# Kernel tuning notes

Hardware: AMD Instinct MI355X
Metric: run time of the kernel (lower is better)

The kernel has to match this reference:

```python
import jax, jax.numpy as jnp
import numpy as np

T, H, E, F, K, FS = 2048, 2048, 64, 512, 8, 512


def setup_inputs() -> dict:
    key = jax.random.key(0)
    ks = jax.random.split(key, 6)
    s = 0.02
    return {
        "hidden_states": jax.random.normal(ks[0], (T, H), jnp.float32),
        # merged gate: E router logits + 1 shared-expert gate logit
        "W_gate": jax.random.normal(ks[1], (H, E + 1), jnp.float32) * s,
        # per-expert merged gate_up proj: [E, H, 2F]
        "W_gate_up": jax.random.normal(ks[2], (E, H, 2 * F), jnp.float32) * s,
        "W_down": jax.random.normal(ks[3], (E, F, H), jnp.float32) * s,
        # shared expert
        "Ws_gate_up": jax.random.normal(ks[4], (H, 2 * FS), jnp.float32) * s,
        "Ws_down": jax.random.normal(ks[5], (FS, H), jnp.float32) * s,
    }


def reference(hidden_states, W_gate, W_gate_up, W_down, Ws_gate_up, Ws_down):
    x = hidden_states  # [T, H]
    logits_all = x @ W_gate                      # [T, E+1]
    router_logits = logits_all[:, :E]
    shared_gate_logit = logits_all[:, E:]        # [T, 1]

    # FusedMoE routing: softmax -> top_k -> renormalize (norm_topk_prob=True)
    probs = jax.nn.softmax(router_logits.astype(jnp.float32), axis=-1)
    topk_w, topk_idx = jax.lax.top_k(probs, K)   # [T, K]
    topk_w = topk_w / jnp.sum(topk_w, axis=-1, keepdims=True)
    # dense combine weights [T, E] (zero for unselected experts)
    combine = jnp.zeros((T, E), probs.dtype).at[
        jnp.arange(T)[:, None], topk_idx].set(topk_w)

    # grouped expert GEMMs (dense reference: every expert sees all tokens,
    # combine-weights zero-out unrouted pairs)
    gu = jnp.einsum('th,ehf->etf', x, W_gate_up)   # [E, T, 2F]
    g, u = jnp.split(gu, 2, axis=-1)
    act = jax.nn.silu(g) * u                       # [E, T, F]
    # apply combine weight before down-proj to avoid [E, T, H] intermediate
    act = act * combine.T[:, :, None].astype(act.dtype)
    routed = jnp.einsum('etf,efh->th', act, W_down)  # [T, H]

    # shared expert (Qwen3NextMLP with sigmoid expert_gate)
    sgu = x @ Ws_gate_up                           # [T, 2FS]
    sg, su = jnp.split(sgu, 2, axis=-1)
    shared = (jax.nn.silu(sg) * su) @ Ws_down      # [T, H]
    shared = jax.nn.sigmoid(shared_gate_logit) * shared

    return shared + routed.astype(x.dtype)
```

## Files before the change

### kernel.cpp

```cpp
#include <hip/hip_runtime.h>
#include <hip/hip_bf16.h>
#include <math.h>

#define T_TOK 2048
#define H_DIM 2048
#define E_NUM 64
#define F_DIM 512
#define K_TOP 8
#define FS_DIM 512
#define NROWS (T_TOK * K_TOP)

typedef __attribute__((ext_vector_type(8))) short short8v;
typedef __attribute__((ext_vector_type(4))) float f32x4;

static __device__ __forceinline__ unsigned short f2bf(float f) {
    unsigned int u = __float_as_uint(f);
    u += 0x7fff + ((u >> 16) & 1);
    return (unsigned short)(u >> 16);
}

#define BCHUNK(row, k8) ((((k8) ^ ((row) + ((row) >> 3)))) & 7)
#define ASWZ(row) (((row) + ((row) >> 3)) & 7)

typedef const unsigned int __attribute__((address_space(1))) gu32;
typedef unsigned int __attribute__((address_space(3))) lu32;
#define GLDS16(gsrc, ldst) \
    __builtin_amdgcn_global_load_lds((gu32*)(gsrc), (lu32*)(ldst), 16, 0, 0)

__global__ __launch_bounds__(256) void cvt_bf16_kernel(
    const float* __restrict__ in, unsigned short* __restrict__ out, int n8)
{
    int i = blockIdx.x * 256 + threadIdx.x;
    if (i < n8) {
        const float4* p = (const float4*)(in + (size_t)i * 8);
        float4 v0 = p[0], v1 = p[1];
        ushort4 a = make_ushort4(f2bf(v0.x), f2bf(v0.y), f2bf(v0.z), f2bf(v0.w));
        ushort4 b = make_ushort4(f2bf(v1.x), f2bf(v1.y), f2bf(v1.z), f2bf(v1.w));
        ushort4* q = (ushort4*)(out + (size_t)i * 8);
        q[0] = a; q[1] = b;
    }
}

__global__ __launch_bounds__(64) void router_kernel(
    const float* __restrict__ x, const float* __restrict__ Wg,
    int* __restrict__ topk_idx, float* __restrict__ topk_w,
    float* __restrict__ sgate, int* __restrict__ counts)
{
    const int t = blockIdx.x;
    const int lane = threadIdx.x;
    const float* xr = x + (size_t)t * H_DIM;

    float a0 = 0.f, a1 = 0.f, a2 = 0.f, a3 = 0.f;
    for (int h = 0; h < H_DIM; h += 4) {
        float4 xv = *(const float4*)&xr[h];
        a0 += xv.x * Wg[(h + 0) * 65 + lane];
        a1 += xv.y * Wg[(h + 1) * 65 + lane];
        a2 += xv.z * Wg[(h + 2) * 65 + lane];
        a3 += xv.w * Wg[(h + 3) * 65 + lane];
    }
    float logit = (a0 + a1) + (a2 + a3);

    float a64 = 0.f;
    for (int h = lane; h < H_DIM; h += 64) a64 += xr[h] * Wg[h * 65 + 64];
#pragma unroll
    for (int off = 32; off >= 1; off >>= 1) a64 += __shfl_xor(a64, off);

    float v = logit;
    float selv[K_TOP]; int seli[K_TOP];
#pragma unroll
    for (int k = 0; k < K_TOP; ++k) {
        float mv = v; int mi = lane;
#pragma unroll
        for (int off = 32; off >= 1; off >>= 1) {
            float ov = __shfl_xor(mv, off);
            int   oi = __shfl_xor(mi, off);
            if (ov > mv || (ov == mv && oi < mi)) { mv = ov; mi = oi; }
        }
        selv[k] = mv; seli[k] = mi;
        if (lane == mi) v = -INFINITY;
    }

    if (lane == 0) {
        float m = selv[0];
        float w[K_TOP]; float s = 0.f;
#pragma unroll
        for (int k = 0; k < K_TOP; ++k) { w[k] = __expf(selv[k] - m); s += w[k]; }
        float inv = 1.f / s;
#pragma unroll
        for (int k = 0; k < K_TOP; ++k) {
            topk_idx[t * K_TOP + k] = seli[k];
            topk_w[t * K_TOP + k] = w[k] * inv;
            atomicAdd(&counts[seli[k]], 1);
        }
        sgate[t] = 1.f / (1.f + __expf(-a64));
    }
}

__global__ __launch_bounds__(256) void bucket_kernel(
    const int* __restrict__ topk_idx, const float* __restrict__ topk_w,
    const int* __restrict__ counts, int* __restrict__ offsets,
    int* __restrict__ bucket_tok, float* __restrict__ bucket_w)
{
    const int e = blockIdx.x, thr = threadIdx.x;
    __shared__ int cnt[256];
    __shared__ int base_s;
    const int q0 = thr * 64;
    int c = 0;
    for (int q = 0; q < 64; ++q) c += (topk_idx[q0 + q] == e) ? 1 : 0;
    cnt[thr] = c;
    __syncthreads();
    if (thr == 0) {
        int off = 0;
        for (int i = 0; i < e; ++i) off += counts[i];
        offsets[e] = off;
        base_s = off;
        int run = 0;
        for (int i = 0; i < 256; ++i) { int tval = cnt[i]; cnt[i] = run; run += tval; }
    }
    __syncthreads();
    int pos = base_s + cnt[thr];
    for (int q = 0; q < 64; ++q) {
        int pp = q0 + q;
        if (topk_idx[pp] == e) {
            bucket_tok[pos] = pp >> 3;
            bucket_w[pos] = topk_w[pp];
            ++pos;
        }
    }
}

template<bool ROUTED>
__global__ __launch_bounds__(256, 2) void gu_mfma_kernel(
    const unsigned short* __restrict__ xb,
    const float* __restrict__ Wall,
    const int* __restrict__ counts, const int* __restrict__ offsets,
    const int* __restrict__ bucket_tok, const float* __restrict__ bucket_w,
    unsigned short* __restrict__ actout)
{
    constexpr int BM = 128;
    __shared__ __align__(16) unsigned short As[2][BM * 64];
    __shared__ __align__(16) unsigned short Bs[2][128 * 64];
    __shared__ int   toksS[BM];
    __shared__ float twsS[BM];

    const int tid  = threadIdx.x;
    const int lane = tid & 63;
    const int wid  = tid >> 6;
    const int wm = wid >> 1, wn = wid & 1;
    const int lrow = lane & 15, lhi = lane >> 4;

    int cblk, ne, base;
    const float* W;
    if (ROUTED) {
        int nw = (blockIdx.x & 7) * ((int)gridDim.x >> 3) + (blockIdx.x >> 3);
        int e = nw >> 3; cblk = nw & 7;
        ne = counts[e]; base = offsets[e];
        W = Wall + (size_t)e * H_DIM * (2 * F_DIM);
    } else {
        cblk = blockIdx.x;
        ne = T_TOK; base = 0;
        W = Wall;
    }
    const int c0 = cblk * 64;

    const int n4 = (tid & 31) * 4;
    const int kq = (tid >> 5) * 8;
    const int grp = n4 >> 5;
    const int srccol = c0 + (grp >> 1) * 32 + (n4 & 31) + ((grp & 1) ? F_DIM : 0);
    int wrB[4];
#pragma unroll
    for (int cc = 0; cc < 4; ++cc) {
        int n = n4 + cc;
        wrB[cc] = n * 64 + BCHUNK(n, kq >> 3) * 8;
    }
    int rdB[4][2];
#pragma unroll
    for (int fn = 0; fn < 4; ++fn) {
        int r = wn * 64 + fn * 16 + lrow;
#pragma unroll
        for (int ks = 0; ks < 2; ++ks) {
            int kc = ks * 4 + lhi;
            rdB[fn][ks] = r * 64 + BCHUNK(r, kc) * 8;
        }
    }
    int rdA[4][2];
#pragma unroll
    for (int fm = 0; fm < 4; ++fm) {
        int arow = wm * 64 + fm * 16 + lrow;
#pragma unroll
        for (int ks = 0; ks < 2; ++ks) {
            int kc = ks * 4 + lhi;
            rdA[fm][ks] = arow * 64 + ((kc ^ ASWZ(arow)) & 7) * 8;
        }
    }
    const int NT = H_DIM / 64;

    const int m0_beg = ROUTED ? 0 : blockIdx.y * BM;
    const int m0_end = ROUTED ? ne : m0_beg + BM;

    for (int m0 = m0_beg; m0 < m0_end; m0 += BM) {
        __syncthreads();
        if (tid < BM) {
            int idx = m0 + tid; bool v = idx < ne;
            if (ROUTED) {
                toksS[tid] = v ? bucket_tok[base + idx] : bucket_tok[base];
                twsS[tid]  = v ? bucket_w[base + idx] : 0.f;
            } else {
                toksS[tid] = v ? idx : (T_TOK - 1);
                twsS[tid]  = 1.f;
            }
        }
        __syncthreads();

        int asrc[4];
#pragma unroll
        for (int i = 0; i < 4; ++i) {
            int row = wid * 32 + i * 8 + (lane >> 3);
            asrc[i] = toksS[row] * H_DIM + (((lane & 7) ^ ASWZ(row)) << 3);
        }

        f32x4 acc[4][4];
#pragma unroll
        for (int i = 0; i < 4; ++i)
#pragma unroll
            for (int j = 0; j < 4; ++j) acc[i][j] = (f32x4){0.f, 0.f, 0.f, 0.f};

        float4 bq[8];
#pragma unroll
        for (int j = 0; j < 8; ++j)
            bq[j] = *(const float4*)&W[(size_t)(kq + j) * (2 * F_DIM) + srccol];
#pragma unroll
        for (int cc = 0; cc < 4; ++cc) {
            short8v pk;
#pragma unroll
            for (int j = 0; j < 8; ++j)
                pk[j] = (short)f2bf(((const float*)&bq[j])[cc]);
            *(short8v*)&Bs[0][wrB[cc]] = pk;
        }
#pragma unroll
        for (int j = 0; j < 8; ++j)
            bq[j] = *(const float4*)&W[(size_t)(64 + kq + j) * (2 * F_DIM) + srccol];
#pragma unroll
        for (int i = 0; i < 4; ++i)
            GLDS16(xb + asrc[i], &As[0][(wid * 32 + i * 8) * 64]);
        __syncthreads();

        for (int kt = 0; kt < NT; ++kt) {
            const int k0 = kt * 64;
            if (kt + 1 < NT) {
#pragma unroll
                for (int i = 0; i < 4; ++i)
                    GLDS16(xb + asrc[i] + k0 + 64, &As[(kt + 1) & 1][(wid * 32 + i * 8) * 64]);
                unsigned short* nB = Bs[(kt + 1) & 1];
#pragma unroll
                for (int cc = 0; cc < 4; ++cc) {
                    short8v pk;
#pragma unroll
                    for (int j = 0; j < 8; ++j)
                        pk[j] = (short)f2bf(((const float*)&bq[j])[cc]);
                    *(short8v*)&nB[wrB[cc]] = pk;
                }
                int knx = (kt + 2 < NT) ? (k0 + 128) : (k0 + 64);
#pragma unroll
                for (int j = 0; j < 8; ++j)
                    bq[j] = *(const float4*)&W[(size_t)(knx + kq + j) * (2 * F_DIM) + srccol];
            }
            __builtin_amdgcn_sched_barrier(0);
            const unsigned short* A_ = As[kt & 1];
            const unsigned short* B_ = Bs[kt & 1];
#pragma unroll
            for (int ks = 0; ks < 2; ++ks) {
                short8v bf[4];
#pragma unroll
                for (int fn = 0; fn < 4; ++fn) bf[fn] = *(const short8v*)&B_[rdB[fn][ks]];
#pragma unroll
                for (int fm = 0; fm < 4; ++fm) {
                    short8v af = *(const short8v*)&A_[rdA[fm][ks]];
#pragma unroll
                    for (int fn = 0; fn < 4; ++fn)
                        acc[fm][fn] = __builtin_amdgcn_mfma_f32_16x16x32_bf16(
                            af, bf[fn], acc[fm][fn], 0, 0, 0);
                }
            }
            __syncthreads();
        }

#pragma unroll
        for (int fm = 0; fm < 4; ++fm) {
#pragma unroll
            for (int p = 0; p < 2; ++p) {
                const int acol = c0 + wn * 32 + p * 16 + lrow;
#pragma unroll
                for (int i = 0; i < 4; ++i) {
                    int ml = wm * 64 + fm * 16 + lhi * 4 + i;
                    int idx = m0 + ml;
                    if (idx < ne) {
                        float gv = acc[fm][p][i], uv = acc[fm][p + 2][i];
                        float sg = gv / (1.f + __expf(-gv));
                        float val = sg * uv * twsS[ml];
                        size_t orow = ROUTED ? (size_t)(base + idx) : (size_t)idx;
                        actout[orow * F_DIM + acol] = f2bf(val);
                    }
                }
            }
        }
    }
}

template<bool ROUTED>
__global__ __launch_bounds__(256, 2) void down_mfma_kernel(
    const unsigned short* __restrict__ actb,
    const float* __restrict__ Wall,
    const int* __restrict__ counts, const int* __restrict__ offsets,
    const int* __restrict__ bucket_tok, const float* __restrict__ sgate,
    float* __restrict__ out)
{
    constexpr int BM = 128;
    __shared__ __align__(16) unsigned short As[2][BM * 64];
    __shared__ __align__(16) unsigned short Bs[2][128 * 64];
    __shared__ int   toksS[BM];
    __shared__ float sgS[BM];

    const int tid  = threadIdx.x;
    const int lane = tid & 63;
    const int wid  = tid >> 6;
    const int wm = wid >> 1, wn = wid & 1;
    const int lrow = lane & 15, lhi = lane >> 4;

    int cblk, ne, base;
    const float* W;
    if (ROUTED) {
        int nw = (blockIdx.x & 7) * ((int)gridDim.x >> 3) + (blockIdx.x >> 3);
        int e = nw >> 4; cblk = nw & 15;
        ne = counts[e]; base = offsets[e];
        W = Wall + (size_t)e * F_DIM * H_DIM;
    } else {
        cblk = blockIdx.x;
        ne = T_TOK; base = 0;
        W = Wall;
    }
    const int c0 = cblk * 128;

    const int n4 = (tid & 31) * 4;
    const int kq = (tid >> 5) * 8;
    const int srccol = c0 + n4;
    int wrB[4];
#pragma unroll
    for (int cc = 0; cc < 4; ++cc) {
        int n = n4 + cc;
        wrB[cc] = n * 64 + BCHUNK(n, kq >> 3) * 8;
    }
    int rdB[4][2];
#pragma unroll
    for (int fn = 0; fn < 4; ++fn) {
        int r = wn * 64 + fn * 16 + lrow;
#pragma unroll
        for (int ks = 0; ks < 2; ++ks) {
            int kc = ks * 4 + lhi;
            rdB[fn][ks] = r * 64 + BCHUNK(r, kc) * 8;
        }
    }
    int rdA[4][2];
#pragma unroll
    for (int fm = 0; fm < 4; ++fm) {
        int arow = wm * 64 + fm * 16 + lrow;
#pragma unroll
        for (int ks = 0; ks < 2; ++ks) {
            int kc = ks * 4 + lhi;
            rdA[fm][ks] = arow * 64 + ((kc ^ ASWZ(arow)) & 7) * 8;
        }
    }
    const int NT = F_DIM / 64;

    const int m0_beg = ROUTED ? 0 : blockIdx.y * BM;
    const int m0_end = ROUTED ? ne : m0_beg + BM;

    for (int m0 = m0_beg; m0 < m0_end; m0 += BM) {
        __syncthreads();
        if (tid < BM) {
            int idx = m0 + tid;
            if (ROUTED) {
                toksS[tid] = (idx < ne) ? bucket_tok[base + idx] : 0;
            } else {
                sgS[tid] = sgate[(idx < ne) ? idx : (T_TOK - 1)];
            }
        }
        __syncthreads();

        int asrc[4];
#pragma unroll
        for (int i = 0; i < 4; ++i) {
            int row = wid * 32 + i * 8 + (lane >> 3);
            int grow = ROUTED ? min(base + m0 + row, NROWS - 1)
                              : min(m0 + row, T_TOK - 1);
            asrc[i] = grow * F_DIM + (((lane & 7) ^ ASWZ(row)) << 3);
        }

        f32x4 acc[4][4];
#pragma unroll
        for (int i = 0; i < 4; ++i)
#pragma unroll
            for (int j = 0; j < 4; ++j) acc[i][j] = (f32x4){0.f, 0.f, 0.f, 0.f};

        float4 bq[8];
#pragma unroll
        for (int j = 0; j < 8; ++j)
            bq[j] = *(const float4*)&W[(size_t)(kq + j) * H_DIM + srccol];
#pragma unroll
        for (int cc = 0; cc < 4; ++cc) {
            short8v pk;
#pragma unroll
            for (int j = 0; j < 8; ++j)
                pk[j] = (short)f2bf(((const float*)&bq[j])[cc]);
            *(short8v*)&Bs[0][wrB[cc]] = pk;
        }
#pragma unroll
        for (int j = 0; j < 8; ++j)
            bq[j] = *(const float4*)&W[(size_t)(64 + kq + j) * H_DIM + srccol];
#pragma unroll
        for (int i = 0; i < 4; ++i)
            GLDS16(actb + asrc[i], &As[0][(wid * 32 + i * 8) * 64]);
        __syncthreads();

        for (int kt = 0; kt < NT; ++kt) {
            const int k0 = kt * 64;
            if (kt + 1 < NT) {
#pragma unroll
                for (int i = 0; i < 4; ++i)
                    GLDS16(actb + asrc[i] + k0 + 64, &As[(kt + 1) & 1][(wid * 32 + i * 8) * 64]);
                unsigned short* nB = Bs[(kt + 1) & 1];
#pragma unroll
                for (int cc = 0; cc < 4; ++cc) {
                    short8v pk;
#pragma unroll
                    for (int j = 0; j < 8; ++j)
                        pk[j] = (short)f2bf(((const float*)&bq[j])[cc]);
                    *(short8v*)&nB[wrB[cc]] = pk;
                }
                int knx = (kt + 2 < NT) ? (k0 + 128) : (k0 + 64);
#pragma unroll
                for (int j = 0; j < 8; ++j)
                    bq[j] = *(const float4*)&W[(size_t)(knx + kq + j) * H_DIM + srccol];
            }
            __builtin_amdgcn_sched_barrier(0);
            const unsigned short* A_ = As[kt & 1];
            const unsigned short* B_ = Bs[kt & 1];
#pragma unroll
            for (int ks = 0; ks < 2; ++ks) {
                short8v bf[4];
#pragma unroll
                for (int fn = 0; fn < 4; ++fn) bf[fn] = *(const short8v*)&B_[rdB[fn][ks]];
#pragma unroll
                for (int fm = 0; fm < 4; ++fm) {
                    short8v af = *(const short8v*)&A_[rdA[fm][ks]];
#pragma unroll
                    for (int fn = 0; fn < 4; ++fn)
                        acc[fm][fn] = __builtin_amdgcn_mfma_f32_16x16x32_bf16(
                            af, bf[fn], acc[fm][fn], 0, 0, 0);
                }
            }
            __syncthreads();
        }

#pragma unroll
        for (int fm = 0; fm < 4; ++fm) {
#pragma unroll
            for (int fn = 0; fn < 4; ++fn) {
                int col = c0 + wn * 64 + fn * 16 + lrow;
#pragma unroll
                for (int i = 0; i < 4; ++i) {
                    int ml = wm * 64 + fm * 16 + lhi * 4 + i;
                    int idx = m0 + ml;
                    if (idx < ne) {
                        if (ROUTED)
                            atomicAdd(&out[(size_t)toksS[ml] * H_DIM + col], acc[fm][fn][i]);
                        else
                            out[(size_t)idx * H_DIM + col] = sgS[ml] * acc[fm][fn][i];
                    }
                }
            }
        }
    }
}

extern "C" void kernel_launch(void* const* d_in, const int* in_sizes, int n_in,
                              void* d_out, int out_size, void* d_ws, size_t ws_size,
                              hipStream_t stream) {
    const float* x    = (const float*)d_in[0];
    const float* Wg   = (const float*)d_in[1];
    const float* Wgu  = (const float*)d_in[2];
    const float* Wd   = (const float*)d_in[3];
    const float* Wsgu = (const float*)d_in[4];
    const float* Wsd  = (const float*)d_in[5];
    float* out = (float*)d_out;

    char* p = (char*)d_ws;
    auto alloc = [&](size_t bytes) {
        char* r = p;
        p += (bytes + 255) & ~(size_t)255;
        return r;
    };
    int*   topk_idx   = (int*)  alloc((size_t)T_TOK * K_TOP * sizeof(int));
    float* topk_w     = (float*)alloc((size_t)T_TOK * K_TOP * sizeof(float));
    float* sgate      = (float*)alloc((size_t)T_TOK * sizeof(float));
    int*   counts     = (int*)  alloc((size_t)E_NUM * sizeof(int));
    int*   offsets    = (int*)  alloc((size_t)E_NUM * sizeof(int));
    int*   bucket_tok = (int*)  alloc((size_t)NROWS * sizeof(int));
    float* bucket_w   = (float*)alloc((size_t)NROWS * sizeof(float));
    unsigned short* xb    = (unsigned short*)alloc((size_t)T_TOK * H_DIM * 2);
    unsigned short* act_r = (unsigned short*)alloc((size_t)NROWS * F_DIM * 2);
    unsigned short* act_s = (unsigned short*)alloc((size_t)T_TOK * FS_DIM * 2);

    hipMemsetAsync(counts, 0, E_NUM * sizeof(int), stream);
    cvt_bf16_kernel<<<(T_TOK * H_DIM / 8 + 255) / 256, 256, 0, stream>>>(x, xb, T_TOK * H_DIM / 8);
    router_kernel<<<T_TOK, 64, 0, stream>>>(x, Wg, topk_idx, topk_w, sgate, counts);
    bucket_kernel<<<E_NUM, 256, 0, stream>>>(topk_idx, topk_w, counts, offsets, bucket_tok, bucket_w);

    gu_mfma_kernel<true><<<8 * E_NUM, 256, 0, stream>>>(
        xb, Wgu, counts, offsets, bucket_tok, bucket_w, act_r);
    gu_mfma_kernel<false><<<dim3(8, T_TOK / 128), 256, 0, stream>>>(
        xb, Wsgu, counts, offsets, bucket_tok, bucket_w, act_s);

    down_mfma_kernel<false><<<dim3(16, T_TOK / 128), 256, 0, stream>>>(
        act_s, Wsd, counts, offsets, bucket_tok, sgate, out);
    down_mfma_kernel<true><<<16 * E_NUM, 256, 0, stream>>>(
        act_r, Wd, counts, offsets, bucket_tok, sgate, out);
}
```

Baseline: 705.7 us.

## Merge shared and routed expert GEMMs into single launches per stage

```diff
diff --git a/kernel.cpp b/kernel.cpp
--- a/kernel.cpp
+++ b/kernel.cpp
@@ -129,13 +129,12 @@
     }
 }
 
-template<bool ROUTED>
 __global__ __launch_bounds__(256, 2) void gu_mfma_kernel(
     const unsigned short* __restrict__ xb,
-    const float* __restrict__ Wall,
+    const float* __restrict__ Wgu, const float* __restrict__ Wsgu,
     const int* __restrict__ counts, const int* __restrict__ offsets,
     const int* __restrict__ bucket_tok, const float* __restrict__ bucket_w,
-    unsigned short* __restrict__ actout)
+    unsigned short* __restrict__ act_r, unsigned short* __restrict__ act_s)
 {
     constexpr int BM = 128;
     __shared__ __align__(16) unsigned short As[2][BM * 64];
@@ -149,17 +148,20 @@
     const int wm = wid >> 1, wn = wid & 1;
     const int lrow = lane & 15, lhi = lane >> 4;
 
-    int cblk, ne, base;
+    const int nw  = (blockIdx.x & 7) * 80 + (blockIdx.x >> 3);
+    const int cblk = nw & 7;
+    const int eu   = nw >> 3;
+    const bool sh  = (eu >= E_NUM);
+    int ne, base, m0_beg, m0_end;
     const float* W;
-    if (ROUTED) {
-        int nw = (blockIdx.x & 7) * ((int)gridDim.x >> 3) + (blockIdx.x >> 3);
-        int e = nw >> 3; cblk = nw & 7;
-        ne = counts[e]; base = offsets[e];
-        W = Wall + (size_t)e * H_DIM * (2 * F_DIM);
+    if (sh) {
+        ne = T_TOK; base = 0;
+        m0_beg = (eu - E_NUM) * BM; m0_end = m0_beg + BM;
+        W = Wsgu;
     } else {
-        cblk = blockIdx.x;
-        ne = T_TOK; base = 0;
-        W = Wall;
+        ne = counts[eu]; base = offsets[eu];
+        m0_beg = 0; m0_end = ne;
+        W = Wgu + (size_t)eu * H_DIM * (2 * F_DIM);
     }
     const int c0 = cblk * 64;
 
@@ -195,19 +197,14 @@
     }
     const int NT = H_DIM / 64;
 
-    const int m0_beg = ROUTED ? 0 : blockIdx.y * BM;
-    const int m0_end = ROUTED ? ne : m0_beg + BM;
-
     for (int m0 = m0_beg; m0 < m0_end; m0 += BM) {
         __syncthreads();
         if (tid < BM) {
             int idx = m0 + tid; bool v = idx < ne;
-            if (ROUTED) {
+            if (sh) { toksS[tid] = v ? idx : (T_TOK - 1); twsS[tid] = 1.f; }
+            else {
                 toksS[tid] = v ? bucket_tok[base + idx] : bucket_tok[base];
                 twsS[tid]  = v ? bucket_w[base + idx] : 0.f;
-            } else {
-                toksS[tid] = v ? idx : (T_TOK - 1);
-                twsS[tid]  = 1.f;
             }
         }
         __syncthreads();
@@ -298,8 +295,8 @@
                         float gv = acc[fm][p][i], uv = acc[fm][p + 2][i];
                         float sg = gv / (1.f + __expf(-gv));
                         float val = sg * uv * twsS[ml];
-                        size_t orow = ROUTED ? (size_t)(base + idx) : (size_t)idx;
-                        actout[orow * F_DIM + acol] = f2bf(val);
+                        if (sh) act_s[(size_t)idx * F_DIM + acol] = f2bf(val);
+                        else    act_r[(size_t)(base + idx) * F_DIM + acol] = f2bf(val);
                     }
                 }
             }
@@ -307,10 +304,10 @@
     }
 }
 
-template<bool ROUTED>
 __global__ __launch_bounds__(256, 2) void down_mfma_kernel(
-    const unsigned short* __restrict__ actb,
-    const float* __restrict__ Wall,
+    const unsigned short* __restrict__ act_r,
+    const unsigned short* __restrict__ act_s,
+    const float* __restrict__ Wd, const float* __restrict__ Wsd,
     const int* __restrict__ counts, const int* __restrict__ offsets,
     const int* __restrict__ bucket_tok, const float* __restrict__ sgate,
     float* __restrict__ out)
@@ -327,17 +324,21 @@
     const int wm = wid >> 1, wn = wid & 1;
     const int lrow = lane & 15, lhi = lane >> 4;
 
-    int cblk, ne, base;
+    const int nw  = (blockIdx.x & 7) * 160 + (blockIdx.x >> 3);
+    const int cblk = nw & 15;
+    const int eu   = nw >> 4;
+    const bool sh  = (eu >= E_NUM);
+    int ne, base, m0_beg, m0_end;
     const float* W;
-    if (ROUTED) {
-        int nw = (blockIdx.x & 7) * ((int)gridDim.x >> 3) + (blockIdx.x >> 3);
-        int e = nw >> 4; cblk = nw & 15;
-        ne = counts[e]; base = offsets[e];
-        W = Wall + (size_t)e * F_DIM * H_DIM;
+    const unsigned short* actb;
+    if (sh) {
+        ne = T_TOK; base = 0;
+        m0_beg = (eu - E_NUM) * BM; m0_end = m0_beg + BM;
+        W = Wsd; actb = act_s;
     } else {
-        cblk = blockIdx.x;
-        ne = T_TOK; base = 0;
-        W = Wall;
+        ne = counts[eu]; base = offsets[eu];
+        m0_beg = 0; m0_end = ne;
+        W = Wd + (size_t)eu * F_DIM * H_DIM; actb = act_r;
     }
     const int c0 = cblk * 128;
 
@@ -372,18 +373,12 @@
     }
     const int NT = F_DIM / 64;
 
-    const int m0_beg = ROUTED ? 0 : blockIdx.y * BM;
-    const int m0_end = ROUTED ? ne : m0_beg + BM;
-
     for (int m0 = m0_beg; m0 < m0_end; m0 += BM) {
         __syncthreads();
         if (tid < BM) {
             int idx = m0 + tid;
-            if (ROUTED) {
-                toksS[tid] = (idx < ne) ? bucket_tok[base + idx] : 0;
-            } else {
-                sgS[tid] = sgate[(idx < ne) ? idx : (T_TOK - 1)];
-            }
+            if (sh) sgS[tid] = sgate[(idx < ne) ? idx : (T_TOK - 1)];
+            else    toksS[tid] = (idx < ne) ? bucket_tok[base + idx] : 0;
         }
         __syncthreads();
 
@@ -391,8 +386,8 @@
 #pragma unroll
         for (int i = 0; i < 4; ++i) {
             int row = wid * 32 + i * 8 + (lane >> 3);
-            int grow = ROUTED ? min(base + m0 + row, NROWS - 1)
-                              : min(m0 + row, T_TOK - 1);
+            int grow = sh ? min(m0 + row, T_TOK - 1)
+                          : min(base + m0 + row, NROWS - 1);
             asrc[i] = grow * F_DIM + (((lane & 7) ^ ASWZ(row)) << 3);
         }
 
@@ -472,10 +467,10 @@
                     int ml = wm * 64 + fm * 16 + lhi * 4 + i;
                     int idx = m0 + ml;
                     if (idx < ne) {
-                        if (ROUTED)
+                        if (sh)
+                            atomicAdd(&out[(size_t)idx * H_DIM + col], sgS[ml] * acc[fm][fn][i]);
+                        else
                             atomicAdd(&out[(size_t)toksS[ml] * H_DIM + col], acc[fm][fn][i]);
-                        else
-                            out[(size_t)idx * H_DIM + col] = sgS[ml] * acc[fm][fn][i];
                     }
                 }
             }
@@ -512,17 +507,14 @@
     unsigned short* act_s = (unsigned short*)alloc((size_t)T_TOK * FS_DIM * 2);
 
     hipMemsetAsync(counts, 0, E_NUM * sizeof(int), stream);
+    hipMemsetAsync(out, 0, (size_t)T_TOK * H_DIM * sizeof(float), stream);
     cvt_bf16_kernel<<<(T_TOK * H_DIM / 8 + 255) / 256, 256, 0, stream>>>(x, xb, T_TOK * H_DIM / 8);
     router_kernel<<<T_TOK, 64, 0, stream>>>(x, Wg, topk_idx, topk_w, sgate, counts);
     bucket_kernel<<<E_NUM, 256, 0, stream>>>(topk_idx, topk_w, counts, offsets, bucket_tok, bucket_w);
 
-    gu_mfma_kernel<true><<<8 * E_NUM, 256, 0, stream>>>(
-        xb, Wgu, counts, offsets, bucket_tok, bucket_w, act_r);
-    gu_mfma_kernel<false><<<dim3(8, T_TOK / 128), 256, 0, stream>>>(
-        xb, Wsgu, counts, offsets, bucket_tok, bucket_w, act_s);
-
-    down_mfma_kernel<false><<<dim3(16, T_TOK / 128), 256, 0, stream>>>(
-        act_s, Wsd, counts, offsets, bucket_tok, sgate, out);
-    down_mfma_kernel<true><<<16 * E_NUM, 256, 0, stream>>>(
-        act_r, Wd, counts, offsets, bucket_tok, sgate, out);
-}
+    gu_mfma_kernel<<<8 * 80, 256, 0, stream>>>(
+        xb, Wgu, Wsgu, counts, offsets, bucket_tok, bucket_w, act_r, act_s);
+
+    down_mfma_kernel<<<16 * 80, 256, 0, stream>>>(
+        act_r, act_s, Wd, Wsd, counts, offsets, bucket_tok, sgate, out);
+}
```

Measured after the change: 757.7 us. 7.4% more time.
